# Performance work log

Hardware: AMD Instinct MI355X
Metric: run time of the kernel (lower is better)

The kernel has to match this reference:

```python
import jax, jax.numpy as jnp
import numpy as np

B, CIN, P, NCLS = 1024, 200, 16, 16
# (in_c, out_c, kernel, stride, pad) per involution layer
LAYERS = [(CIN, 64, 2, 2, 0), (64, 128, 2, 2, 0), (128, 256, 3, 1, 1)]
BN_EPS = 1e-5


def _involution(x, W_init, W_red, gamma, beta, W_span, k, s, p):
    # Reich-style Involution2d, groups=1, reduce_ratio=1, bias=False
    Bn = x.shape[0]
    out_c = W_init.shape[0]
    # initial 1x1 mapping (in_c != out_c for every layer here)
    xi = jnp.einsum('oc,bchw->bohw', W_init, x)
    # unfold -> [B, out_c*k*k, Ho, Wo] (channel-major patch ordering = torch unfold)
    patches = jax.lax.conv_general_dilated_patches(xi, (k, k), (s, s), [(p, p), (p, p)])
    Ho, Wo = patches.shape[-2], patches.shape[-1]
    patches = patches.reshape(Bn, out_c, k * k, Ho, Wo)
    # kernel-generation branch: AvgPool(stride) -> 1x1 reduce -> BN+ReLU -> 1x1 span
    if s > 1:
        Bx, C, H, W = x.shape
        xp = x.reshape(Bx, C, H // s, s, W // s, s).mean(axis=(3, 5))
    else:
        xp = x
    r = jnp.einsum('oc,bchw->bohw', W_red, xp)
    mean = r.mean(axis=(0, 2, 3), keepdims=True)
    var = r.var(axis=(0, 2, 3), keepdims=True)
    r = gamma[None, :, None, None] * (r - mean) * jax.lax.rsqrt(var + BN_EPS) + beta[None, :, None, None]
    r = jax.nn.relu(r)
    kern = jnp.einsum('ko,bohw->bkhw', W_span, r)  # [B, k*k, Ho, Wo]
    # dynamic per-pixel kernel applied to unfolded patches, summed over k*k
    return jnp.einsum('bkhw,bokhw->bohw', kern, patches)


def setup_inputs() -> dict:
    key = jax.random.key(0)
    ks = jax.random.split(key, 20)
    inp = {'x': jax.random.normal(ks[0], (B, CIN, P, P), dtype=jnp.float32)}
    i = 1
    for li, (cin, cout, k, s, p) in enumerate(LAYERS, start=1):
        inp[f'W_init{li}'] = jax.random.normal(ks[i], (cout, cin), dtype=jnp.float32) * (1.0 / np.sqrt(cin)); i += 1
        inp[f'W_red{li}'] = jax.random.normal(ks[i], (cout, cin), dtype=jnp.float32) * (1.0 / np.sqrt(cin)); i += 1
        inp[f'gamma{li}'] = jnp.ones((cout,), dtype=jnp.float32)
        inp[f'beta{li}'] = jnp.zeros((cout,), dtype=jnp.float32)
        inp[f'W_span{li}'] = jax.random.normal(ks[i], (k * k, cout), dtype=jnp.float32) * (1.0 / np.sqrt(cout)); i += 1
    feat = 256 * 4 * 4  # 16 ->8 ->4 ->4 spatial, 256 channels
    inp['W_fc'] = jax.random.normal(ks[i], (NCLS, feat), dtype=jnp.float32) * (1.0 / np.sqrt(feat))
    inp['b_fc'] = jnp.zeros((NCLS,), dtype=jnp.float32)
    return inp


def reference(x, W_init1, W_red1, gamma1, beta1, W_span1,
              W_init2, W_red2, gamma2, beta2, W_span2,
              W_init3, W_red3, gamma3, beta3, W_span3,
              W_fc, b_fc):
    h = _involution(x, W_init1, W_red1, gamma1, beta1, W_span1, 2, 2, 0)
    h = _involution(h, W_init2, W_red2, gamma2, beta2, W_span2, 2, 2, 0)
    h = _involution(h, W_init3, W_red3, gamma3, beta3, W_span3, 3, 1, 1)
    h = h.reshape(h.shape[0], -1)
    return h @ W_fc.T + b_fc
```

## Files before the change

kernel.cpp:

```cpp
#include <hip/hip_runtime.h>


typedef __attribute__((ext_vector_type(8))) short short8v;
typedef __attribute__((ext_vector_type(4))) float f32x4;

__device__ __forceinline__ unsigned short f2bf_rne(float x) {
    unsigned u = __float_as_uint(x);
    unsigned r = u + 0x7FFFu + ((u >> 16) & 1u);
    return (unsigned short)(r >> 16);
}
__device__ __forceinline__ float bf2f(unsigned short h) {
    return __uint_as_float(((unsigned)h) << 16);
}

static constexpr size_t OFF_SUM1  = 0;
static constexpr size_t OFF_SQS1  = 512;
static constexpr size_t OFF_SUM2  = 1024;
static constexpr size_t OFF_SQS2  = 2048;
static constexpr size_t OFF_SUM3  = 3072;
static constexpr size_t OFF_SQS3  = 5120;
static constexpr size_t OFF_WCAT2 = 25600;
static constexpr size_t OFF_WCAT3 = 41984;
static constexpr size_t OFF_XI1   = 108416;
static constexpr size_t OFF_RPRE1 = 16885632;
static constexpr size_t OFF_XI2   = 21079936;
static constexpr size_t OFF_RPRE2 = 29468544;
static constexpr size_t OFF_APKH  = OFF_XI2;
static constexpr size_t OFF_APKL  = OFF_XI2 + 14336;

__global__ void prep_all(const float* __restrict__ wi2, const float* __restrict__ wr2,
                         const float* __restrict__ wi3, const float* __restrict__ wr3,
                         float* __restrict__ ws) {
    int e = blockIdx.x * 256 + threadIdx.x;
    if (e < 7168) { ws[e] = 0.f; return; }
    if (e < 25600 || e >= 107520) return;
    const float* wi; const float* wr; float* wt; int cin, cout;
    if (e < 41984) { e -= 25600; wi = wi2; wr = wr2; wt = ws + OFF_WCAT2; cin = 64;  cout = 128; }
    else           { e -= 41984; wi = wi3; wr = wr3; wt = ws + OFF_WCAT3; cin = 128; cout = 256; }
    int M = 2 * cout, c = e / M, m = e % M;
    wt[e] = (m < cout) ? wi[m * cin + c] : wr[(m - cout) * cin + c];
}

__global__ void prep_apk(const float* __restrict__ wi1, const float* __restrict__ wr1,
                         unsigned short* __restrict__ ah, unsigned short* __restrict__ al) {
    int e = blockIdx.x * 256 + threadIdx.x;
    if (e >= 28672) return;
    int v  = e & 7;
    int l  = (e >> 3) & 63;
    int mt = (e >> 9) & 7;
    int ck = e >> 12;
    int c = 32 * ck + ((l >> 4) << 3) + v;
    int m = 16 * mt + (l & 15);
    float wv = 0.f;
    if (c < 200) wv = (m < 64) ? wi1[m * 200 + c] : wr1[(m - 64) * 200 + c];
    unsigned short h = f2bf_rne(wv);
    ah[e] = h;
    al[e] = f2bf_rne(wv - bf2f(h));
}

__global__ __launch_bounds__(512) void p1_l1_mfma(
    const float* __restrict__ x,
    const unsigned short* __restrict__ aHiG,
    const unsigned short* __restrict__ aLoG,
    float* __restrict__ xi,
    float* __restrict__ rpre,
    float* __restrict__ ssum, float* __restrict__ ssqs)
{
    __shared__ __align__(16) unsigned short bHi[8192];
    __shared__ __align__(16) unsigned short bLo[8192];
    const int tid = threadIdx.x, b = blockIdx.x;
    const int lane = tid & 63, w = tid >> 6;
    const int shard = (b & 7) * 64;
    const float* xb = x + (size_t)b * 200 * 256;

    f32x4 acc[16];
    #pragma unroll
    for (int i = 0; i < 16; ++i) acc[i] = f32x4{0.f, 0.f, 0.f, 0.f};

    float v0[8], v1[8];
    auto load_slot = [&](int s, int c0, float* v) {
        int l = s & 63;
        int n = (((s >> 6) << 4)) | (l & 15);
        int cb = c0 + ((l >> 4) << 3);
        #pragma unroll
        for (int j = 0; j < 8; ++j) {
            int c = cb + j;
            v[j] = (c < 200) ? xb[c * 256 + n] : 0.f;
        }
    };
    auto write_slot = [&](int s, const float* v) {
        unsigned short h[8], g[8];
        #pragma unroll
        for (int j = 0; j < 8; ++j) {
            h[j] = f2bf_rne(v[j]);
            g[j] = f2bf_rne(v[j] - bf2f(h[j]));
        }
        uint4 ph, pl;
        ph.x = (unsigned)h[0] | ((unsigned)h[1] << 16);
        ph.y = (unsigned)h[2] | ((unsigned)h[3] << 16);
        ph.z = (unsigned)h[4] | ((unsigned)h[5] << 16);
        ph.w = (unsigned)h[6] | ((unsigned)h[7] << 16);
        pl.x = (unsigned)g[0] | ((unsigned)g[1] << 16);
        pl.y = (unsigned)g[2] | ((unsigned)g[3] << 16);
        pl.z = (unsigned)g[4] | ((unsigned)g[5] << 16);
        pl.w = (unsigned)g[6] | ((unsigned)g[7] << 16);
        *(uint4*)(bHi + (size_t)s * 8) = ph;
        *(uint4*)(bLo + (size_t)s * 8) = pl;
    };

    load_slot(tid, 0, v0);
    load_slot(tid + 512, 0, v1);

    for (int ck = 0; ck < 7; ++ck) {
        write_slot(tid, v0);
        write_slot(tid + 512, v1);
        __syncthreads();
        if (ck < 6) {
            load_slot(tid, 32 * (ck + 1), v0);
            load_slot(tid + 512, 32 * (ck + 1), v1);
        }
        const size_t abase = ((size_t)(ck * 8 + w) * 64 + lane) * 8;
        short8v aH = *(const short8v*)(aHiG + abase);
        short8v aL = *(const short8v*)(aLoG + abase);
        #pragma unroll
        for (int nt = 0; nt < 16; ++nt) {
            short8v bH = *(const short8v*)(bHi + ((size_t)(nt * 64 + lane)) * 8);
            short8v bL = *(const short8v*)(bLo + ((size_t)(nt * 64 + lane)) * 8);
            acc[nt] = __builtin_amdgcn_mfma_f32_16x16x32_bf16(aH, bH, acc[nt], 0, 0, 0);
            acc[nt] = __builtin_amdgcn_mfma_f32_16x16x32_bf16(aH, bL, acc[nt], 0, 0, 0);
            acc[nt] = __builtin_amdgcn_mfma_f32_16x16x32_bf16(aL, bH, acc[nt], 0, 0, 0);
        }
        __syncthreads();
    }

    const int g = lane >> 4, col = lane & 15;
    if (w < 4) {
        float* xr = xi + ((size_t)b * 64 + 16 * w + 4 * g) * 256 + col;
        #pragma unroll
        for (int r = 0; r < 4; ++r)
            #pragma unroll
            for (int nt = 0; nt < 16; ++nt)
                xr[(size_t)r * 256 + nt * 16] = acc[nt][r];
    } else {
        #pragma unroll
        for (int r = 0; r < 4; ++r) {
            const int mr = 16 * (w - 4) + 4 * g + r;
            float pv[8], s1 = 0.f, s2 = 0.f;
            #pragma unroll
            for (int ph = 0; ph < 8; ++ph) {
                float a0 = acc[2 * ph][r], a1 = acc[2 * ph + 1][r];
                float p = 0.25f * (a0 + __shfl_xor(a0, 1) + a1 + __shfl_xor(a1, 1));
                pv[ph] = p; s1 += p; s2 += p * p;
            }
            if ((col & 1) == 0) {
                float* rp = rpre + ((size_t)b * 64 + mr) * 64 + (col >> 1);
                #pragma unroll
                for (int ph = 0; ph < 8; ++ph) rp[ph * 8] = pv[ph];
            }
            s1 += __shfl_xor(s1, 2); s2 += __shfl_xor(s2, 2);
            s1 += __shfl_xor(s1, 4); s2 += __shfl_xor(s2, 4);
            s1 += __shfl_xor(s1, 8); s2 += __shfl_xor(s2, 8);
            if (col == 0) { atomicAdd(ssum + shard + mr, s1); atomicAdd(ssqs + shard + mr, s2); }
        }
    }
}

__global__ __launch_bounds__(256) void f2_kernel(
    const float* __restrict__ xi1,
    const float* __restrict__ rpre1,
    const float* __restrict__ ssum1, const float* __restrict__ ssqs1,
    const float* __restrict__ gamma1, const float* __restrict__ beta1,
    const float* __restrict__ wspan1,
    const float* __restrict__ wT2,
    float* __restrict__ xi2,
    float* __restrict__ rpre2,
    float* __restrict__ ssum2, float* __restrict__ ssqs2)
{
    __shared__ float sc[64], sh[64];
    __shared__ float kl[4 * 64];
    __shared__ float rws[4096];
    __shared__ float Xl[4096];
    const int tid = threadIdx.x, b = blockIdx.x;
    const int shard = (b & 7) * 128;

    if (tid < 64) {
        float s1v = 0.f, s2v = 0.f;
        #pragma unroll
        for (int s = 0; s < 8; ++s) { s1v += ssum1[s * 64 + tid]; s2v += ssqs1[s * 64 + tid]; }
        float mean = s1v * (1.f / 65536.f);
        float var  = s2v * (1.f / 65536.f) - mean * mean;
        float s    = gamma1[tid] * rsqrtf(var + 1e-5f);
        sc[tid] = s; sh[tid] = beta1[tid] - mean * s;
    }
    __syncthreads();
    const float* rp1 = rpre1 + (size_t)b * 4096;
    for (int e = tid; e < 4096; e += 256) {
        int o = e >> 6;
        rws[e] = fmaxf(fmaf(sc[o], rp1[e], sh[o]), 0.f);
    }
    __syncthreads();
    {
        int kk = tid >> 6, q = tid & 63;
        float s = 0.f;
        #pragma unroll
        for (int o = 0; o < 64; ++o)
            s = fmaf(wspan1[kk * 64 + o], rws[(o << 6) + q], s);
        kl[tid] = s;
    }
    __syncthreads();
    const float* xb1 = xi1 + (size_t)b * 64 * 256;
    for (int e = tid; e < 4096; e += 256) {
        int o = e >> 6, q = e & 63, ho = q >> 3, wo = q & 7;
        const float* p = xb1 + ((size_t)(o * 16 + 2 * ho)) * 16 + 2 * wo;
        float2 t  = *(const float2*)p;
        float2 bo = *(const float2*)(p + 16);
        Xl[e] = kl[q] * t.x + kl[64 + q] * t.y + kl[128 + q] * bo.x + kl[192 + q] * bo.y;
    }
    __syncthreads();

    const int tn = tid & 7, tm = tid >> 3;
    float acc[8][8];
    #pragma unroll
    for (int i = 0; i < 8; ++i)
        #pragma unroll
        for (int j = 0; j < 8; ++j) acc[i][j] = 0.f;

    for (int c0 = 0; c0 < 64; c0 += 16) {
        for (int e = tid * 4; e < 4096; e += 1024)
            *(float4*)(rws + e) = *(const float4*)(wT2 + (size_t)c0 * 256 + e);
        __syncthreads();
        #pragma unroll
        for (int c = 0; c < 16; ++c) {
            float4 xa = *(const float4*)(Xl + (c0 + c) * 64 + tn * 4);
            float4 xc = *(const float4*)(Xl + (c0 + c) * 64 + 32 + tn * 4);
            float4 wa = *(const float4*)(rws + c * 256 + tm * 4);
            float4 wb = *(const float4*)(rws + c * 256 + 128 + tm * 4);
            float xf[8] = {xa.x, xa.y, xa.z, xa.w, xc.x, xc.y, xc.z, xc.w};
            float wf[8] = {wa.x, wa.y, wa.z, wa.w, wb.x, wb.y, wb.z, wb.w};
            #pragma unroll
            for (int i = 0; i < 8; ++i)
                #pragma unroll
                for (int j = 0; j < 8; ++j)
                    acc[i][j] = fmaf(wf[i], xf[j], acc[i][j]);
        }
        __syncthreads();
    }

    const int gr = tm * 4;
    #pragma unroll
    for (int i = 0; i < 4; ++i) {
        float* dst = xi2 + ((size_t)b * 128 + gr + i) * 64 + tn * 4;
        float4 v0 = {acc[i][0], acc[i][1], acc[i][2], acc[i][3]};
        float4 v1 = {acc[i][4], acc[i][5], acc[i][6], acc[i][7]};
        *(float4*)dst = v0;
        *(float4*)(dst + 32) = v1;
    }
    const bool val = (tn & 2) == 0;
    #pragma unroll
    for (int i = 4; i < 8; ++i) {
        const int mr = gr + i - 4;
        float hp0 = acc[i][0] + acc[i][1], hp1 = acc[i][2] + acc[i][3];
        float hp2 = acc[i][4] + acc[i][5], hp3 = acc[i][6] + acc[i][7];
        float p0 = 0.25f * (hp0 + __shfl_xor(hp0, 2));
        float p1 = 0.25f * (hp1 + __shfl_xor(hp1, 2));
        float p2 = 0.25f * (hp2 + __shfl_xor(hp2, 2));
        float p3 = 0.25f * (hp3 + __shfl_xor(hp3, 2));
        float s1 = val ? (p0 + p1 + p2 + p3) : 0.f;
        float s2 = val ? (p0 * p0 + p1 * p1 + p2 * p2 + p3 * p3) : 0.f;
        if (val) {
            const int wo = (tn & 1) * 2, ho = tn >> 2;
            float* rp = rpre2 + ((size_t)b * 128 + mr) * 16;
            *(float2*)(rp + ho * 4 + wo) = float2{p0, p1};
            *(float2*)(rp + (2 + ho) * 4 + wo) = float2{p2, p3};
        }
        #pragma unroll
        for (int off = 1; off <= 4; off <<= 1) {
            s1 += __shfl_xor(s1, off); s2 += __shfl_xor(s2, off);
        }
        if (tn == 0) { atomicAdd(ssum2 + shard + mr, s1); atomicAdd(ssqs2 + shard + mr, s2); }
    }
}

__global__ __launch_bounds__(256) void f3_kernel(
    const float* __restrict__ xi2,
    const float* __restrict__ rpre2,
    const float* __restrict__ ssum2, const float* __restrict__ ssqs2,
    const float* __restrict__ gamma2, const float* __restrict__ beta2,
    const float* __restrict__ wspan2,
    const float* __restrict__ wT3,
    float* __restrict__ xi3,
    float* __restrict__ rpre3,
    float* __restrict__ ssum3, float* __restrict__ ssqs3)
{
    __shared__ float sc[128], sh[128];
    __shared__ float kl[4 * 16];
    __shared__ float rws[8192];
    __shared__ float Xl[2048];
    const int tid = threadIdx.x, b = blockIdx.x;
    const int shard = (b & 7) * 256;

    if (tid < 128) {
        float s1v = 0.f, s2v = 0.f;
        #pragma unroll
        for (int s = 0; s < 8; ++s) { s1v += ssum2[s * 128 + tid]; s2v += ssqs2[s * 128 + tid]; }
        float mean = s1v * (1.f / 16384.f);
        float var  = s2v * (1.f / 16384.f) - mean * mean;
        float s    = gamma2[tid] * rsqrtf(var + 1e-5f);
        sc[tid] = s; sh[tid] = beta2[tid] - mean * s;
    }
    __syncthreads();
    const float* rp2 = rpre2 + (size_t)b * 2048;
    for (int e = tid; e < 2048; e += 256) {
        int o = e >> 4;
        rws[e] = fmaxf(fmaf(sc[o], rp2[e], sh[o]), 0.f);
    }
    __syncthreads();
    if (tid < 64) {
        int kk = tid >> 4, q = tid & 15;
        float s = 0.f;
        #pragma unroll
        for (int o = 0; o < 128; ++o)
            s = fmaf(wspan2[kk * 128 + o], rws[(o << 4) + q], s);
        kl[tid] = s;
    }
    __syncthreads();
    const float* xb2 = xi2 + (size_t)b * 128 * 64;
    for (int e = tid; e < 2048; e += 256) {
        int o = e >> 4, q = e & 15, ho = q >> 2, wo = q & 3;
        const float* p = xb2 + ((size_t)(o * 8 + 2 * ho)) * 8 + 2 * wo;
        float2 t  = *(const float2*)p;
        float2 bo = *(const float2*)(p + 8);
        Xl[e] = kl[q] * t.x + kl[16 + q] * t.y + kl[32 + q] * bo.x + kl[48 + q] * bo.y;
    }
    __syncthreads();

    const int tn = tid & 3, tm = tid >> 2;
    float acc[8][4];
    #pragma unroll
    for (int i = 0; i < 8; ++i)
        #pragma unroll
        for (int j = 0; j < 4; ++j) acc[i][j] = 0.f;

    for (int c0 = 0; c0 < 128; c0 += 16) {
        for (int e = tid * 4; e < 8192; e += 1024)
            *(float4*)(rws + e) = *(const float4*)(wT3 + (size_t)c0 * 512 + e);
        __syncthreads();
        #pragma unroll
        for (int c = 0; c < 16; ++c) {
            float4 xa = *(const float4*)(Xl + (c0 + c) * 16 + tn * 4);
            float4 wa = *(const float4*)(rws + c * 512 + tm * 4);
            float4 wb = *(const float4*)(rws + c * 512 + 256 + tm * 4);
            float xfv[4] = {xa.x, xa.y, xa.z, xa.w};
            float wf[8] = {wa.x, wa.y, wa.z, wa.w, wb.x, wb.y, wb.z, wb.w};
            #pragma unroll
            for (int i = 0; i < 8; ++i)
                #pragma unroll
                for (int j = 0; j < 4; ++j)
                    acc[i][j] = fmaf(wf[i], xfv[j], acc[i][j]);
        }
        __syncthreads();
    }

    const int gr = tm * 4;
    #pragma unroll
    for (int i = 0; i < 4; ++i) {
        float4 v0 = {acc[i][0], acc[i][1], acc[i][2], acc[i][3]};
        *(float4*)(xi3 + ((size_t)b * 256 + gr + i) * 16 + tn * 4) = v0;
    }
    #pragma unroll
    for (int i = 4; i < 8; ++i) {
        const int mr = gr + i - 4;
        float4 v0 = {acc[i][0], acc[i][1], acc[i][2], acc[i][3]};
        *(float4*)(rpre3 + ((size_t)b * 256 + mr) * 16 + tn * 4) = v0;
        float s1 = acc[i][0] + acc[i][1] + acc[i][2] + acc[i][3];
        float s2 = acc[i][0] * acc[i][0] + acc[i][1] * acc[i][1]
                 + acc[i][2] * acc[i][2] + acc[i][3] * acc[i][3];
        s1 += __shfl_xor(s1, 1); s2 += __shfl_xor(s2, 1);
        s1 += __shfl_xor(s1, 2); s2 += __shfl_xor(s2, 2);
        if (tn == 0) { atomicAdd(ssum3 + shard + mr, s1); atomicAdd(ssqs3 + shard + mr, s2); }
    }
}

__global__ __launch_bounds__(256) void f4_kernel(
    const float* __restrict__ xi3,
    const float* __restrict__ rpre3,
    const float* __restrict__ ssum3, const float* __restrict__ ssqs3,
    const float* __restrict__ gamma3, const float* __restrict__ beta3,
    const float* __restrict__ wspan3,
    const float* __restrict__ wfc,
    const float* __restrict__ bfc,
    float* __restrict__ out)
{
    __shared__ float sc[256], sh[256];
    __shared__ float kl[9 * 16];
    __shared__ float xil[4096];
    __shared__ float rh[4096];
    __shared__ float red[4][16];
    const int tid = threadIdx.x, b = blockIdx.x;

    {
        float s1v = 0.f, s2v = 0.f;
        #pragma unroll
        for (int s = 0; s < 8; ++s) { s1v += ssum3[s * 256 + tid]; s2v += ssqs3[s * 256 + tid]; }
        float mean = s1v * (1.f / 16384.f);
        float var  = s2v * (1.f / 16384.f) - mean * mean;
        float s    = gamma3[tid] * rsqrtf(var + 1e-5f);
        sc[tid] = s; sh[tid] = beta3[tid] - mean * s;
    }
    const float* xb3 = xi3 + (size_t)b * 4096;
    for (int e = tid; e < 1024; e += 256)
        ((float4*)xil)[e] = ((const float4*)xb3)[e];
    __syncthreads();

    const float* rp3 = rpre3 + (size_t)b * 4096;
    for (int e = tid; e < 4096; e += 256) {
        int o = e >> 4;
        rh[e] = fmaxf(fmaf(sc[o], rp3[e], sh[o]), 0.f);
    }
    __syncthreads();
    if (tid < 144) {
        int kk = tid >> 4, q = tid & 15;
        float s = 0.f;
        #pragma unroll
        for (int o = 0; o < 256; ++o)
            s = fmaf(wspan3[kk * 256 + o], rh[(o << 4) + q], s);
        kl[tid] = s;
    }
    __syncthreads();
    for (int e = tid; e < 4096; e += 256) {
        int o = e >> 4, q = e & 15, ho = q >> 2, wo = q & 3;
        float v = 0.f;
        const float* xo = xil + (o << 4);
        #pragma unroll
        for (int ki = 0; ki < 3; ++ki) {
            int h = ho + ki - 1;
            if (h < 0 || h >= 4) continue;
            #pragma unroll
            for (int kj = 0; kj < 3; ++kj) {
                int w = wo + kj - 1;
                if (w < 0 || w >= 4) continue;
                v = fmaf(kl[(ki * 3 + kj) * 16 + q], xo[h * 4 + w], v);
            }
        }
        rh[e] = v;
    }
    __syncthreads();

    float acc[16];
    #pragma unroll
    for (int n = 0; n < 16; ++n) acc[n] = 0.f;
    for (int i = 0; i < 16; ++i) {
        int f = tid + i * 256;
        float hv = rh[f];
        #pragma unroll
        for (int n = 0; n < 16; ++n)
            acc[n] = fmaf(hv, wfc[n * 4096 + f], acc[n]);
    }
    #pragma unroll
    for (int n = 0; n < 16; ++n) {
        float v = acc[n];
        #pragma unroll
        for (int off = 1; off < 64; off <<= 1) v += __shfl_xor(v, off);
        acc[n] = v;
    }
    const int wave = tid >> 6, lane = tid & 63;
    if (lane == 0) {
        #pragma unroll
        for (int n = 0; n < 16; ++n) red[wave][n] = acc[n];
    }
    __syncthreads();
    if (tid < 16)
        out[(size_t)b * 16 + tid] =
            red[0][tid] + red[1][tid] + red[2][tid] + red[3][tid] + bfc[tid];
}

extern "C" void kernel_launch(void* const* d_in, const int* in_sizes, int n_in,
                              void* d_out, int out_size, void* d_ws, size_t ws_size,
                              hipStream_t stream) {
    const float* x    = (const float*)d_in[0];
    const float* Wi1  = (const float*)d_in[1];
    const float* Wr1  = (const float*)d_in[2];
    const float* g1   = (const float*)d_in[3];
    const float* be1  = (const float*)d_in[4];
    const float* Wsp1 = (const float*)d_in[5];
    const float* Wi2  = (const float*)d_in[6];
    const float* Wr2  = (const float*)d_in[7];
    const float* g2   = (const float*)d_in[8];
    const float* be2  = (const float*)d_in[9];
    const float* Wsp2 = (const float*)d_in[10];
    const float* Wi3  = (const float*)d_in[11];
    const float* Wr3  = (const float*)d_in[12];
    const float* g3   = (const float*)d_in[13];
    const float* be3  = (const float*)d_in[14];
    const float* Wsp3 = (const float*)d_in[15];
    const float* Wfc  = (const float*)d_in[16];
    const float* bfc  = (const float*)d_in[17];
    float* out = (float*)d_out;
    float* ws  = (float*)d_ws;

    float* sum1 = ws + OFF_SUM1; float* sqs1 = ws + OFF_SQS1;
    float* sum2 = ws + OFF_SUM2; float* sqs2 = ws + OFF_SQS2;
    float* sum3 = ws + OFF_SUM3; float* sqs3 = ws + OFF_SQS3;
    float* wcat2 = ws + OFF_WCAT2;
    float* wcat3 = ws + OFF_WCAT3;
    float* xi1   = ws + OFF_XI1;
    float* rpre1 = ws + OFF_RPRE1;
    float* xi2   = ws + OFF_XI2;
    float* rpre2 = ws + OFF_RPRE2;
    float* xi3   = ws + OFF_XI1;
    float* rpre3 = ws + OFF_RPRE1;
    unsigned short* apkh = (unsigned short*)(ws + OFF_APKH);
    unsigned short* apkl = (unsigned short*)(ws + OFF_APKL);

    prep_all<<<420, 256, 0, stream>>>(Wi2, Wr2, Wi3, Wr3, ws);
    prep_apk<<<112, 256, 0, stream>>>(Wi1, Wr1, apkh, apkl);

    p1_l1_mfma<<<1024, 512, 0, stream>>>(x, apkh, apkl, xi1, rpre1, sum1, sqs1);

    f2_kernel<<<1024, 256, 0, stream>>>(xi1, rpre1, sum1, sqs1, g1, be1, Wsp1,
                                        wcat2, xi2, rpre2, sum2, sqs2);

    f3_kernel<<<1024, 256, 0, stream>>>(xi2, rpre2, sum2, sqs2, g2, be2, Wsp2,
                                        wcat3, xi3, rpre3, sum3, sqs3);

    f4_kernel<<<1024, 256, 0, stream>>>(xi3, rpre3, sum3, sqs3, g3, be3, Wsp3,
                                        Wfc, bfc, out);
}
```

Baseline: 544.4 us.

## Use split-bf16 MFMA for layer 2 and 3 channel-mixing GEMMs

Replaces the FP32 FMA register-tiled GEMMs in f2 and f3 with bf16 MFMA 16x16x32 using a hi/lo split (three MFMAs per tile) to approximate FP32 accuracy. Weights for both layers are prepacked into MFMA fragment layout in the prep kernel, and each block converts its involution output into hi/lo bf16 fragments in LDS. The epilogues are rewritten for the MFMA output layout, including pooling and BN statistics. The aim is to cut ALU time in these GEMMs, at the cost of extra conversion work and a small precision change.

```diff
diff --git a/kernel.cpp b/kernel.cpp
--- a/kernel.cpp
+++ b/kernel.cpp
@@ -19,8 +19,10 @@
 static constexpr size_t OFF_SQS2  = 2048;
 static constexpr size_t OFF_SUM3  = 3072;
 static constexpr size_t OFF_SQS3  = 5120;
-static constexpr size_t OFF_WCAT2 = 25600;
-static constexpr size_t OFF_WCAT3 = 41984;
+static constexpr size_t OFF_A2H   = 7168;
+static constexpr size_t OFF_A2L   = 15360;
+static constexpr size_t OFF_A3H   = 23552;
+static constexpr size_t OFF_A3L   = 56320;
 static constexpr size_t OFF_XI1   = 108416;
 static constexpr size_t OFF_RPRE1 = 16885632;
 static constexpr size_t OFF_XI2   = 21079936;
@@ -28,34 +30,45 @@
 static constexpr size_t OFF_APKH  = OFF_XI2;
 static constexpr size_t OFF_APKL  = OFF_XI2 + 14336;
 
-__global__ void prep_all(const float* __restrict__ wi2, const float* __restrict__ wr2,
+__global__ void prep_all(float* __restrict__ ws) {
+    int e = blockIdx.x * 256 + threadIdx.x;
+    if (e < 7168) ws[e] = 0.f;
+}
+
+__global__ void prep_apk(const float* __restrict__ wi1, const float* __restrict__ wr1,
+                         const float* __restrict__ wi2, const float* __restrict__ wr2,
                          const float* __restrict__ wi3, const float* __restrict__ wr3,
-                         float* __restrict__ ws) {
+                         unsigned short* __restrict__ a1h, unsigned short* __restrict__ a1l,
+                         unsigned short* __restrict__ a2h, unsigned short* __restrict__ a2l,
+                         unsigned short* __restrict__ a3h, unsigned short* __restrict__ a3l) {
     int e = blockIdx.x * 256 + threadIdx.x;
-    if (e < 7168) { ws[e] = 0.f; return; }
-    if (e < 25600 || e >= 107520) return;
-    const float* wi; const float* wr; float* wt; int cin, cout;
-    if (e < 41984) { e -= 25600; wi = wi2; wr = wr2; wt = ws + OFF_WCAT2; cin = 64;  cout = 128; }
-    else           { e -= 41984; wi = wi3; wr = wr3; wt = ws + OFF_WCAT3; cin = 128; cout = 256; }
-    int M = 2 * cout, c = e / M, m = e % M;
-    wt[e] = (m < cout) ? wi[m * cin + c] : wr[(m - cout) * cin + c];
-}
-
-__global__ void prep_apk(const float* __restrict__ wi1, const float* __restrict__ wr1,
-                         unsigned short* __restrict__ ah, unsigned short* __restrict__ al) {
-    int e = blockIdx.x * 256 + threadIdx.x;
-    if (e >= 28672) return;
-    int v  = e & 7;
-    int l  = (e >> 3) & 63;
-    int mt = (e >> 9) & 7;
-    int ck = e >> 12;
-    int c = 32 * ck + ((l >> 4) << 3) + v;
-    int m = 16 * mt + (l & 15);
-    float wv = 0.f;
-    if (c < 200) wv = (m < 64) ? wi1[m * 200 + c] : wr1[(m - 64) * 200 + c];
+    if (e >= 110592) return;
+    float wv; unsigned short* dh; unsigned short* dl; int idx;
+    if (e < 28672) {
+        int v = e & 7, l = (e >> 3) & 63, mt = (e >> 9) & 7, ck = e >> 12;
+        int c = 32 * ck + ((l >> 4) << 3) + v;
+        int m = 16 * mt + (l & 15);
+        wv = 0.f;
+        if (c < 200) wv = (m < 64) ? wi1[m * 200 + c] : wr1[(m - 64) * 200 + c];
+        dh = a1h; dl = a1l; idx = e;
+    } else if (e < 45056) {
+        int e2 = e - 28672;
+        int v = e2 & 7, l = (e2 >> 3) & 63, mt = (e2 >> 9) & 15, ck = e2 >> 13;
+        int c = 32 * ck + ((l >> 4) << 3) + v;
+        int m = 16 * mt + (l & 15);
+        wv = (m < 128) ? wi2[m * 64 + c] : wr2[(m - 128) * 64 + c];
+        dh = a2h; dl = a2l; idx = e2;
+    } else {
+        int e3 = e - 45056;
+        int v = e3 & 7, l = (e3 >> 3) & 63, mt = (e3 >> 9) & 31, ck = e3 >> 14;
+        int c = 32 * ck + ((l >> 4) << 3) + v;
+        int m = 16 * mt + (l & 15);
+        wv = (m < 256) ? wi3[m * 128 + c] : wr3[(m - 256) * 128 + c];
+        dh = a3h; dl = a3l; idx = e3;
+    }
     unsigned short h = f2bf_rne(wv);
-    ah[e] = h;
-    al[e] = f2bf_rne(wv - bf2f(h));
+    dh[idx] = h;
+    dl[idx] = f2bf_rne(wv - bf2f(h));
 }
 
 __global__ __launch_bounds__(512) void p1_l1_mfma(
@@ -171,15 +184,17 @@
     const float* __restrict__ ssum1, const float* __restrict__ ssqs1,
     const float* __restrict__ gamma1, const float* __restrict__ beta1,
     const float* __restrict__ wspan1,
-    const float* __restrict__ wT2,
+    const unsigned short* __restrict__ a2h, const unsigned short* __restrict__ a2l,
     float* __restrict__ xi2,
     float* __restrict__ rpre2,
     float* __restrict__ ssum2, float* __restrict__ ssqs2)
 {
     __shared__ float sc[64], sh[64];
-    __shared__ float kl[4 * 64];
-    __shared__ float rws[4096];
-    __shared__ float Xl[4096];
+    __shared__ float kl[256];
+    __shared__ float rl[4096];
+    __shared__ float Xl[64 * 65];
+    __shared__ __align__(16) unsigned short bH[4096];
+    __shared__ __align__(16) unsigned short bL[4096];
     const int tid = threadIdx.x, b = blockIdx.x;
     const int shard = (b & 7) * 128;
 
@@ -196,7 +211,7 @@
     const float* rp1 = rpre1 + (size_t)b * 4096;
     for (int e = tid; e < 4096; e += 256) {
         int o = e >> 6;
-        rws[e] = fmaxf(fmaf(sc[o], rp1[e], sh[o]), 0.f);
+        rl[e] = fmaxf(fmaf(sc[o], rp1[e], sh[o]), 0.f);
     }
     __syncthreads();
     {
@@ -204,7 +219,7 @@
         float s = 0.f;
         #pragma unroll
         for (int o = 0; o < 64; ++o)
-            s = fmaf(wspan1[kk * 64 + o], rws[(o << 6) + q], s);
+            s = fmaf(wspan1[kk * 64 + o], rl[(o << 6) + q], s);
         kl[tid] = s;
     }
     __syncthreads();
@@ -214,70 +229,99 @@
         const float* p = xb1 + ((size_t)(o * 16 + 2 * ho)) * 16 + 2 * wo;
         float2 t  = *(const float2*)p;
         float2 bo = *(const float2*)(p + 16);
-        Xl[e] = kl[q] * t.x + kl[64 + q] * t.y + kl[128 + q] * bo.x + kl[192 + q] * bo.y;
-    }
-    __syncthreads();
-
-    const int tn = tid & 7, tm = tid >> 3;
-    float acc[8][8];
-    #pragma unroll
-    for (int i = 0; i < 8; ++i)
-        #pragma unroll
-        for (int j = 0; j < 8; ++j) acc[i][j] = 0.f;
-
-    for (int c0 = 0; c0 < 64; c0 += 16) {
-        for (int e = tid * 4; e < 4096; e += 1024)
-            *(float4*)(rws + e) = *(const float4*)(wT2 + (size_t)c0 * 256 + e);
-        __syncthreads();
-        #pragma unroll
-        for (int c = 0; c < 16; ++c) {
-            float4 xa = *(const float4*)(Xl + (c0 + c) * 64 + tn * 4);
-            float4 xc = *(const float4*)(Xl + (c0 + c) * 64 + 32 + tn * 4);
-            float4 wa = *(const float4*)(rws + c * 256 + tm * 4);
-            float4 wb = *(const float4*)(rws + c * 256 + 128 + tm * 4);
-            float xf[8] = {xa.x, xa.y, xa.z, xa.w, xc.x, xc.y, xc.z, xc.w};
-            float wf[8] = {wa.x, wa.y, wa.z, wa.w, wb.x, wb.y, wb.z, wb.w};
-            #pragma unroll
-            for (int i = 0; i < 8; ++i)
+        Xl[o * 65 + q] = kl[q] * t.x + kl[64 + q] * t.y + kl[128 + q] * bo.x + kl[192 + q] * bo.y;
+    }
+    __syncthreads();
+
+    #pragma unroll
+    for (int t = 0; t < 2; ++t) {
+        int s = tid + t * 256;
+        int ck = s >> 8, nt = (s >> 6) & 3, l = s & 63;
+        int ob = ck * 32 + ((l >> 4) << 3), q = nt * 16 + (l & 15);
+        unsigned short h[8], g8[8];
+        #pragma unroll
+        for (int j = 0; j < 8; ++j) {
+            float v = Xl[(ob + j) * 65 + q];
+            h[j] = f2bf_rne(v);
+            g8[j] = f2bf_rne(v - bf2f(h[j]));
+        }
+        uint4 ph, pl;
+        ph.x = (unsigned)h[0] | ((unsigned)h[1] << 16);
+        ph.y = (unsigned)h[2] | ((unsigned)h[3] << 16);
+        ph.z = (unsigned)h[4] | ((unsigned)h[5] << 16);
+        ph.w = (unsigned)h[6] | ((unsigned)h[7] << 16);
+        pl.x = (unsigned)g8[0] | ((unsigned)g8[1] << 16);
+        pl.y = (unsigned)g8[2] | ((unsigned)g8[3] << 16);
+        pl.z = (unsigned)g8[4] | ((unsigned)g8[5] << 16);
+        pl.w = (unsigned)g8[6] | ((unsigned)g8[7] << 16);
+        *(uint4*)(bH + ((size_t)ck * 2048 + (size_t)(nt * 64 + l) * 8)) = ph;
+        *(uint4*)(bL + ((size_t)ck * 2048 + (size_t)(nt * 64 + l) * 8)) = pl;
+    }
+    __syncthreads();
+
+    const int w = tid >> 6, l = tid & 63;
+    f32x4 acc[4][4];
+    #pragma unroll
+    for (int i = 0; i < 4; ++i)
+        #pragma unroll
+        for (int j = 0; j < 4; ++j) acc[i][j] = f32x4{0.f, 0.f, 0.f, 0.f};
+    #pragma unroll
+    for (int ck = 0; ck < 2; ++ck) {
+        #pragma unroll
+        for (int mi = 0; mi < 4; ++mi) {
+            int mt = w + 4 * mi;
+            const size_t ab = ((size_t)(ck * 16 + mt) * 64 + l) * 8;
+            short8v aH = *(const short8v*)(a2h + ab);
+            short8v aL = *(const short8v*)(a2l + ab);
+            #pragma unroll
+            for (int nt = 0; nt < 4; ++nt) {
+                short8v bHv = *(const short8v*)(bH + ((size_t)ck * 2048 + (size_t)(nt * 64 + l) * 8));
+                short8v bLv = *(const short8v*)(bL + ((size_t)ck * 2048 + (size_t)(nt * 64 + l) * 8));
+                acc[mi][nt] = __builtin_amdgcn_mfma_f32_16x16x32_bf16(aH, bHv, acc[mi][nt], 0, 0, 0);
+                acc[mi][nt] = __builtin_amdgcn_mfma_f32_16x16x32_bf16(aH, bLv, acc[mi][nt], 0, 0, 0);
+                acc[mi][nt] = __builtin_amdgcn_mfma_f32_16x16x32_bf16(aL, bHv, acc[mi][nt], 0, 0, 0);
+            }
+        }
+    }
+
+    const int g = l >> 4, c = l & 15;
+    #pragma unroll
+    for (int mi = 0; mi < 2; ++mi) {
+        int mt = w + 4 * mi;
+        #pragma unroll
+        for (int r = 0; r < 4; ++r) {
+            float* dst = xi2 + ((size_t)b * 128 + mt * 16 + 4 * g + r) * 64 + c;
+            #pragma unroll
+            for (int nt = 0; nt < 4; ++nt) dst[nt * 16] = acc[mi][nt][r];
+        }
+    }
+    const bool valid = ((c & 1) == 0) && ((c & 8) == 0);
+    #pragma unroll
+    for (int mi = 2; mi < 4; ++mi) {
+        int mt = w + 4 * mi - 8;
+        #pragma unroll
+        for (int r = 0; r < 4; ++r) {
+            const int mr = mt * 16 + 4 * g + r;
+            float pv[4], s1 = 0.f, s2 = 0.f;
+            #pragma unroll
+            for (int nt = 0; nt < 4; ++nt) {
+                float v = acc[mi][nt][r];
+                float hp = v + __shfl_xor(v, 1);
+                float p = 0.25f * (hp + __shfl_xor(hp, 8));
+                pv[nt] = p; s1 += p; s2 += p * p;
+            }
+            if (valid) {
+                float* rp = rpre2 + ((size_t)b * 128 + mr) * 16 + (c >> 1);
                 #pragma unroll
-                for (int j = 0; j < 8; ++j)
-                    acc[i][j] = fmaf(wf[i], xf[j], acc[i][j]);
-        }
-        __syncthreads();
-    }
-
-    const int gr = tm * 4;
-    #pragma unroll
-    for (int i = 0; i < 4; ++i) {
-        float* dst = xi2 + ((size_t)b * 128 + gr + i) * 64 + tn * 4;
-        float4 v0 = {acc[i][0], acc[i][1], acc[i][2], acc[i][3]};
-        float4 v1 = {acc[i][4], acc[i][5], acc[i][6], acc[i][7]};
-        *(float4*)dst = v0;
-        *(float4*)(dst + 32) = v1;
-    }
-    const bool val = (tn & 2) == 0;
-    #pragma unroll
-    for (int i = 4; i < 8; ++i) {
-        const int mr = gr + i - 4;
-        float hp0 = acc[i][0] + acc[i][1], hp1 = acc[i][2] + acc[i][3];
-        float hp2 = acc[i][4] + acc[i][5], hp3 = acc[i][6] + acc[i][7];
-        float p0 = 0.25f * (hp0 + __shfl_xor(hp0, 2));
-        float p1 = 0.25f * (hp1 + __shfl_xor(hp1, 2));
-        float p2 = 0.25f * (hp2 + __shfl_xor(hp2, 2));
-        float p3 = 0.25f * (hp3 + __shfl_xor(hp3, 2));
-        float s1 = val ? (p0 + p1 + p2 + p3) : 0.f;
-        float s2 = val ? (p0 * p0 + p1 * p1 + p2 * p2 + p3 * p3) : 0.f;
-        if (val) {
-            const int wo = (tn & 1) * 2, ho = tn >> 2;
-            float* rp = rpre2 + ((size_t)b * 128 + mr) * 16;
-            *(float2*)(rp + ho * 4 + wo) = float2{p0, p1};
-            *(float2*)(rp + (2 + ho) * 4 + wo) = float2{p2, p3};
-        }
-        #pragma unroll
-        for (int off = 1; off <= 4; off <<= 1) {
-            s1 += __shfl_xor(s1, off); s2 += __shfl_xor(s2, off);
-        }
-        if (tn == 0) { atomicAdd(ssum2 + shard + mr, s1); atomicAdd(ssqs2 + shard + mr, s2); }
+                for (int nt = 0; nt < 4; ++nt) rp[nt * 4] = pv[nt];
+            }
+            s1 = valid ? s1 : 0.f; s2 = valid ? s2 : 0.f;
+            #pragma unroll
+            for (int off = 1; off <= 8; off <<= 1) {
+                s1 += __shfl_xor(s1, off); s2 += __shfl_xor(s2, off);
+            }
+            if (c == 0) { atomicAdd(ssum2 + shard + mr, s1); atomicAdd(ssqs2 + shard + mr, s2); }
+        }
     }
 }
 
@@ -287,15 +331,17 @@
     const float* __restrict__ ssum2, const float* __restrict__ ssqs2,
     const float* __restrict__ gamma2, const float* __restrict__ beta2,
     const float* __restrict__ wspan2,
-    const float* __restrict__ wT3,
+    const unsigned short* __restrict__ a3h, const unsigned short* __restrict__ a3l,
     float* __restrict__ xi3,
     float* __restrict__ rpre3,
     float* __restrict__ ssum3, float* __restrict__ ssqs3)
 {
     __shared__ float sc[128], sh[128];
-    __shared__ float kl[4 * 16];
-    __shared__ float rws[8192];
-    __shared__ float Xl[2048];
+    __shared__ float kl[64];
+    __shared__ float rl[2048];
+    __shared__ float Xl[128 * 17];
+    __shared__ __align__(16) unsigned short bH[2048];
+    __shared__ __align__(16) unsigned short bL[2048];
     const int tid = threadIdx.x, b = blockIdx.x;
     const int shard = (b & 7) * 256;
 
@@ -312,7 +358,7 @@
     const float* rp2 = rpre2 + (size_t)b * 2048;
     for (int e = tid; e < 2048; e += 256) {
         int o = e >> 4;
-        rws[e] = fmaxf(fmaf(sc[o], rp2[e], sh[o]), 0.f);
+        rl[e] = fmaxf(fmaf(sc[o], rp2[e], sh[o]), 0.f);
     }
     __syncthreads();
     if (tid < 64) {
@@ -320,7 +366,7 @@
         float s = 0.f;
         #pragma unroll
         for (int o = 0; o < 128; ++o)
-            s = fmaf(wspan2[kk * 128 + o], rws[(o << 4) + q], s);
+            s = fmaf(wspan2[kk * 128 + o], rl[(o << 4) + q], s);
         kl[tid] = s;
     }
     __syncthreads();
@@ -330,54 +376,77 @@
         const float* p = xb2 + ((size_t)(o * 8 + 2 * ho)) * 8 + 2 * wo;
         float2 t  = *(const float2*)p;
         float2 bo = *(const float2*)(p + 8);
-        Xl[e] = kl[q] * t.x + kl[16 + q] * t.y + kl[32 + q] * bo.x + kl[48 + q] * bo.y;
-    }
-    __syncthreads();
-
-    const int tn = tid & 3, tm = tid >> 2;
-    float acc[8][4];
-    #pragma unroll
-    for (int i = 0; i < 8; ++i)
-        #pragma unroll
-        for (int j = 0; j < 4; ++j) acc[i][j] = 0.f;
-
-    for (int c0 = 0; c0 < 128; c0 += 16) {
-        for (int e = tid * 4; e < 8192; e += 1024)
-            *(float4*)(rws + e) = *(const float4*)(wT3 + (size_t)c0 * 512 + e);
-        __syncthreads();
-        #pragma unroll
-        for (int c = 0; c < 16; ++c) {
-            float4 xa = *(const float4*)(Xl + (c0 + c) * 16 + tn * 4);
-            float4 wa = *(const float4*)(rws + c * 512 + tm * 4);
-            float4 wb = *(const float4*)(rws + c * 512 + 256 + tm * 4);
-            float xfv[4] = {xa.x, xa.y, xa.z, xa.w};
-            float wf[8] = {wa.x, wa.y, wa.z, wa.w, wb.x, wb.y, wb.z, wb.w};
-            #pragma unroll
-            for (int i = 0; i < 8; ++i)
-                #pragma unroll
-                for (int j = 0; j < 4; ++j)
-                    acc[i][j] = fmaf(wf[i], xfv[j], acc[i][j]);
-        }
-        __syncthreads();
-    }
-
-    const int gr = tm * 4;
-    #pragma unroll
-    for (int i = 0; i < 4; ++i) {
-        float4 v0 = {acc[i][0], acc[i][1], acc[i][2], acc[i][3]};
-        *(float4*)(xi3 + ((size_t)b * 256 + gr + i) * 16 + tn * 4) = v0;
-    }
-    #pragma unroll
-    for (int i = 4; i < 8; ++i) {
-        const int mr = gr + i - 4;
-        float4 v0 = {acc[i][0], acc[i][1], acc[i][2], acc[i][3]};
-        *(float4*)(rpre3 + ((size_t)b * 256 + mr) * 16 + tn * 4) = v0;
-        float s1 = acc[i][0] + acc[i][1] + acc[i][2] + acc[i][3];
-        float s2 = acc[i][0] * acc[i][0] + acc[i][1] * acc[i][1]
-                 + acc[i][2] * acc[i][2] + acc[i][3] * acc[i][3];
-        s1 += __shfl_xor(s1, 1); s2 += __shfl_xor(s2, 1);
-        s1 += __shfl_xor(s1, 2); s2 += __shfl_xor(s2, 2);
-        if (tn == 0) { atomicAdd(ssum3 + shard + mr, s1); atomicAdd(ssqs3 + shard + mr, s2); }
+        Xl[o * 17 + q] = kl[q] * t.x + kl[16 + q] * t.y + kl[32 + q] * bo.x + kl[48 + q] * bo.y;
+    }
+    __syncthreads();
+
+    {
+        int ck = tid >> 6, l = tid & 63;
+        int ob = ck * 32 + ((l >> 4) << 3), q = l & 15;
+        unsigned short h[8], g8[8];
+        #pragma unroll
+        for (int j = 0; j < 8; ++j) {
+            float v = Xl[(ob + j) * 17 + q];
+            h[j] = f2bf_rne(v);
+            g8[j] = f2bf_rne(v - bf2f(h[j]));
+        }
+        uint4 ph, pl;
+        ph.x = (unsigned)h[0] | ((unsigned)h[1] << 16);
+        ph.y = (unsigned)h[2] | ((unsigned)h[3] << 16);
+        ph.z = (unsigned)h[4] | ((unsigned)h[5] << 16);
+        ph.w = (unsigned)h[6] | ((unsigned)h[7] << 16);
+        pl.x = (unsigned)g8[0] | ((unsigned)g8[1] << 16);
+        pl.y = (unsigned)g8[2] | ((unsigned)g8[3] << 16);
+        pl.z = (unsigned)g8[4] | ((unsigned)g8[5] << 16);
+        pl.w = (unsigned)g8[6] | ((unsigned)g8[7] << 16);
+        *(uint4*)(bH + (size_t)tid * 8) = ph;
+        *(uint4*)(bL + (size_t)tid * 8) = pl;
+    }
+    __syncthreads();
+
+    const int w = tid >> 6, l = tid & 63;
+    f32x4 acc[8];
+    #pragma unroll
+    for (int i = 0; i < 8; ++i) acc[i] = f32x4{0.f, 0.f, 0.f, 0.f};
+    #pragma unroll
+    for (int ck = 0; ck < 4; ++ck) {
+        short8v bHv = *(const short8v*)(bH + ((size_t)(ck * 64 + l)) * 8);
+        short8v bLv = *(const short8v*)(bL + ((size_t)(ck * 64 + l)) * 8);
+        #pragma unroll
+        for (int mi = 0; mi < 8; ++mi) {
+            int mt = w + 4 * mi;
+            const size_t ab = ((size_t)(ck * 32 + mt) * 64 + l) * 8;
+            short8v aH = *(const short8v*)(a3h + ab);
+            short8v aL = *(const short8v*)(a3l + ab);
+            acc[mi] = __builtin_amdgcn_mfma_f32_16x16x32_bf16(aH, bHv, acc[mi], 0, 0, 0);
+            acc[mi] = __builtin_amdgcn_mfma_f32_16x16x32_bf16(aH, bLv, acc[mi], 0, 0, 0);
+            acc[mi] = __builtin_amdgcn_mfma_f32_16x16x32_bf16(aL, bHv, acc[mi], 0, 0, 0);
+        }
+    }
+
+    const int g = l >> 4, c = l & 15;
+    #pragma unroll
+    for (int mi = 0; mi < 4; ++mi) {
+        int mt = w + 4 * mi;
+        #pragma unroll
+        for (int r = 0; r < 4; ++r)
+            xi3[((size_t)b * 256 + mt * 16 + 4 * g + r) * 16 + c] = acc[mi][r];
+    }
+    #pragma unroll
+    for (int mi = 4; mi < 8; ++mi) {
+        int mt = w + 4 * mi - 16;
+        #pragma unroll
+        for (int r = 0; r < 4; ++r) {
+            const int mr = mt * 16 + 4 * g + r;
+            float v = acc[mi][r];
+            rpre3[((size_t)b * 256 + mr) * 16 + c] = v;
+            float s1 = v, s2 = v * v;
+            #pragma unroll
+            for (int off = 1; off <= 8; off <<= 1) {
+                s1 += __shfl_xor(s1, off); s2 += __shfl_xor(s2, off);
+            }
+            if (c == 0) { atomicAdd(ssum3 + shard + mr, s1); atomicAdd(ssqs3 + shard + mr, s2); }
+        }
     }
 }
 
@@ -501,27 +570,30 @@
     float* sum1 = ws + OFF_SUM1; float* sqs1 = ws + OFF_SQS1;
     float* sum2 = ws + OFF_SUM2; float* sqs2 = ws + OFF_SQS2;
     float* sum3 = ws + OFF_SUM3; float* sqs3 = ws + OFF_SQS3;
-    float* wcat2 = ws + OFF_WCAT2;
-    float* wcat3 = ws + OFF_WCAT3;
     float* xi1   = ws + OFF_XI1;
     float* rpre1 = ws + OFF_RPRE1;
     float* xi2   = ws + OFF_XI2;
     float* rpre2 = ws + OFF_RPRE2;
     float* xi3   = ws + OFF_XI1;
     float* rpre3 = ws + OFF_RPRE1;
-    unsigned short* apkh = (unsigned short*)(ws + OFF_APKH);
-    unsigned short* apkl = (unsigned short*)(ws + OFF_APKL);
-
-    prep_all<<<420, 256, 0, stream>>>(Wi2, Wr2, Wi3, Wr3, ws);
-    prep_apk<<<112, 256, 0, stream>>>(Wi1, Wr1, apkh, apkl);
-
-    p1_l1_mfma<<<1024, 512, 0, stream>>>(x, apkh, apkl, xi1, rpre1, sum1, sqs1);
+    unsigned short* a1h = (unsigned short*)(ws + OFF_APKH);
+    unsigned short* a1l = (unsigned short*)(ws + OFF_APKL);
+    unsigned short* a2h = (unsigned short*)(ws + OFF_A2H);
+    unsigned short* a2l = (unsigned short*)(ws + OFF_A2L);
+    unsigned short* a3h = (unsigned short*)(ws + OFF_A3H);
+    unsigned short* a3l = (unsigned short*)(ws + OFF_A3L);
+
+    prep_all<<<28, 256, 0, stream>>>(ws);
+    prep_apk<<<432, 256, 0, stream>>>(Wi1, Wr1, Wi2, Wr2, Wi3, Wr3,
+                                      a1h, a1l, a2h, a2l, a3h, a3l);
+
+    p1_l1_mfma<<<1024, 512, 0, stream>>>(x, a1h, a1l, xi1, rpre1, sum1, sqs1);
 
     f2_kernel<<<1024, 256, 0, stream>>>(xi1, rpre1, sum1, sqs1, g1, be1, Wsp1,
-                                        wcat2, xi2, rpre2, sum2, sqs2);
+                                        a2h, a2l, xi2, rpre2, sum2, sqs2);
 
     f3_kernel<<<1024, 256, 0, stream>>>(xi2, rpre2, sum2, sqs2, g2, be2, Wsp2,
-                                        wcat3, xi3, rpre3, sum3, sqs3);
+                                        a3h, a3l, xi3, rpre3, sum3, sqs3);
 
     f4_kernel<<<1024, 256, 0, stream>>>(xi3, rpre3, sum3, sqs3, g3, be3, Wsp3,
                                         Wfc, bfc, out);
```

New measurement: 468.9 us. 1.16x faster.
